# Kernel tuning notes

Hardware: AMD Instinct MI355X
Metric: run time of the kernel (lower is better)

Reference implementation:

```python
import jax, jax.numpy as jnp
import numpy as np

N_NODES = 50000
N_EDGES = 800000
NUM_GRAPHS = 512
EMB = 128
OUT_DIM = 2145 * 2
EPS_BN = 1e-5
EPS_GN = 1e-5


def gat_conv(x, src, dst, W, att_s, att_d, bias, n):
    # PyG GATConv, heads=1: h = x W ; alpha_e = leakyrelu(a_s.h[src] + a_d.h[dst])
    h = x @ W                                   # [N, EMB]
    a_s = h @ att_s                             # [N]
    a_d = h @ att_d                             # [N]
    logits = jax.nn.leaky_relu(a_s[src] + a_d[dst], 0.2)   # [E]
    m = jax.ops.segment_max(logits, dst, num_segments=n)
    ex = jnp.exp(logits - m[dst])
    denom = jax.ops.segment_sum(ex, dst, num_segments=n)
    alpha = ex / (denom[dst] + 1e-16)           # segment softmax over in-edges
    out = jax.ops.segment_sum(alpha[:, None] * h[src], dst, num_segments=n)
    return out + bias


def setup_inputs() -> dict:
    key = jax.random.key(0)
    ks = jax.random.split(key, 16)
    x = jax.random.normal(ks[0], (N_NODES, 1), dtype=jnp.float32)
    edge_index = jax.random.randint(ks[1], (2, N_EDGES), 0, N_NODES, dtype=jnp.int64)
    batch = jnp.sort(jax.random.randint(ks[2], (N_NODES,), 0, NUM_GRAPHS, dtype=jnp.int64))
    edge_attr = jax.random.normal(ks[3], (N_EDGES, 1), dtype=jnp.float32)
    s = 0.1
    return {
        "x": x, "edge_index": edge_index, "batch": batch, "edge_attr": edge_attr,
        "W0": jax.random.normal(ks[4], (1, EMB), dtype=jnp.float32) * s,
        "as0": jax.random.normal(ks[5], (EMB,), dtype=jnp.float32) * s,
        "ad0": jax.random.normal(ks[6], (EMB,), dtype=jnp.float32) * s,
        "b0": jnp.zeros((EMB,), dtype=jnp.float32),
        "W1": jax.random.normal(ks[7], (EMB, EMB), dtype=jnp.float32) * s,
        "as1": jax.random.normal(ks[8], (EMB,), dtype=jnp.float32) * s,
        "ad1": jax.random.normal(ks[9], (EMB,), dtype=jnp.float32) * s,
        "b1": jnp.zeros((EMB,), dtype=jnp.float32),
        "bn_g": jnp.ones((EMB,), dtype=jnp.float32),
        "bn_b": jnp.zeros((EMB,), dtype=jnp.float32),
        "gn_w": jnp.ones((EMB,), dtype=jnp.float32),
        "gn_b": jnp.zeros((EMB,), dtype=jnp.float32),
        "gn_ms": jnp.ones((EMB,), dtype=jnp.float32),
        "Wout": jax.random.normal(ks[10], (2 * EMB, OUT_DIM), dtype=jnp.float32) * s,
        "bout": jnp.zeros((OUT_DIM,), dtype=jnp.float32),
    }


def reference(x, edge_index, batch, edge_attr, W0, as0, ad0, b0, W1, as1, ad1, b1,
              bn_g, bn_b, gn_w, gn_b, gn_ms, Wout, bout):
    n = x.shape[0]
    # PyG GATConv add_self_loops=True
    loops = jnp.arange(n, dtype=edge_index.dtype)
    src = jnp.concatenate([edge_index[0], loops])
    dst = jnp.concatenate([edge_index[1], loops])
    # edge_attr ignored (edge_dim=None in GATConv)

    h = jnp.tanh(gat_conv(x, src, dst, W0, as0, ad0, b0, n))
    # dropout p=0.2 treated as identity (deterministic eval reference)

    # BatchNorm over nodes (training/batch statistics)
    mu = jnp.mean(h, axis=0)
    var = jnp.mean((h - mu) ** 2, axis=0)
    h = bn_g * (h - mu) / jnp.sqrt(var + EPS_BN) + bn_b

    # GraphNorm: per-graph mean-scale normalization
    cnt = jax.ops.segment_sum(jnp.ones((n,), h.dtype), batch, num_segments=NUM_GRAPHS)[:, None]
    gmean = jax.ops.segment_sum(h, batch, num_segments=NUM_GRAPHS) / cnt
    h0 = h - gmean[batch] * gn_ms
    gvar = jax.ops.segment_sum(h0 ** 2, batch, num_segments=NUM_GRAPHS) / cnt
    h = gn_w * h0 / jnp.sqrt(gvar[batch] + EPS_GN) + gn_b

    h = jnp.tanh(gat_conv(h, src, dst, W1, as1, ad1, b1, n))

    # global max + mean pool per graph
    pmax = jax.ops.segment_max(h, batch, num_segments=NUM_GRAPHS)
    pmean = jax.ops.segment_sum(h, batch, num_segments=NUM_GRAPHS) / cnt
    pooled = jnp.concatenate([pmax, pmean], axis=1)   # [G, 2*EMB]
    return pooled @ Wout + bout                        # [G, OUT_DIM]
```

## Files before the change

### kernel.cpp

```cpp
#include <hip/hip_runtime.h>
#include <hip/hip_fp16.h>
#include <math.h>

#define EMB 128
#define NGRAPH 512
#define MAXBUCK 800
#define BCAP 1536
#define CHUNK 8192

typedef _Float16 f16_t;
typedef _Float16 f16x8 __attribute__((ext_vector_type(8)));
typedef float f32x4 __attribute__((ext_vector_type(4)));

__device__ __forceinline__ float leaky(float v){ return v > 0.f ? v : 0.2f*v; }
__device__ __forceinline__ float ftanh(float x){
    float u = __expf(2.f*x);
    return 1.f - 2.f*__builtin_amdgcn_rcpf(u + 1.f);
}
__device__ __forceinline__ float frcp(float x){ return __builtin_amdgcn_rcpf(x); }

__global__ __launch_bounds__(256) void k_misc(const float* W0, const float* as0, const float* ad0,
                                              float* c_sd, const float* W1, f16_t* W1t,
                                              const float* Wout, int OUT, f16_t* WoutT){
    __shared__ f16_t lt[64*68];
    __shared__ float s1[128], s2[128];
    int b = blockIdx.x;
    int t = threadIdx.x;
    if(b < 272){
        int n0 = (b%68)*64, k0 = (b/68)*64;
        #pragma unroll
        for(int j=0;j<16;j++){
            int k_l = (t>>6)*16 + j;
            int n_l = t&63;
            int n = n0+n_l;
            float v = (n < OUT) ? Wout[(size_t)(k0+k_l)*OUT + n] : 0.f;
            lt[n_l*68 + k_l] = (f16_t)v;
        }
        __syncthreads();
        #pragma unroll
        for(int j=0;j<16;j++){
            int n_l = (t>>6)*16 + j;
            int k_l = t&63;
            WoutT[(size_t)(n0+n_l)*256 + k0 + k_l] = lt[n_l*68 + k_l];
        }
    } else if(b < 336){
        int idx = (b-272)*256 + t;
        int n = idx>>7, k = idx&127;
        W1t[n*128+k] = (f16_t)W1[k*128+n];
    } else {
        if(t<128){ float w = W0[t]; s1[t]=w*as0[t]; s2[t]=w*ad0[t]; }
        __syncthreads();
        for(int off=64; off>0; off>>=1){
            if(t<off){ s1[t]+=s1[t+off]; s2[t]+=s2[t+off]; }
            __syncthreads();
        }
        if(t==0){ c_sd[0]=s1[0]; c_sd[1]=s2[0]; }
    }
}

__global__ void k_bcount(const int* dst, int E, int nbuck, int* bcnt){
    __shared__ int h[MAXBUCK];
    int t = threadIdx.x;
    for(int j=t;j<MAXBUCK;j+=512) h[j]=0;
    __syncthreads();
    int stride = gridDim.x*blockDim.x;
    for(int e = blockIdx.x*blockDim.x+t; e<E; e+=stride)
        atomicAdd(&h[dst[e]>>6], 1);
    __syncthreads();
    for(int j=t;j<nbuck;j+=512) if(h[j]) atomicAdd(&bcnt[j], h[j]);
}

__global__ void k_bscan(const int* bcnt, int nbuck, int* bbase, int* bcursor,
                        const int* batch, int N, int* gstart){
    __shared__ int s[1024];
    int t = threadIdx.x;
    int own = (t<nbuck)? bcnt[t] : 0;
    s[t] = own;
    __syncthreads();
    for(int off=1; off<1024; off<<=1){
        int a = (t>=off)? s[t-off] : 0;
        __syncthreads();
        s[t] += a;
        __syncthreads();
    }
    if(t<nbuck){ int ex = s[t]-own; bbase[t]=ex; bcursor[t]=ex; }
    if(t==nbuck-1) bbase[nbuck]=s[t];
    for(int i=t; i<N; i+=1024){
        int b2 = batch[i];
        if(i==0){ for(int g=0;g<=b2;g++) gstart[g]=0; }
        else { int bp=batch[i-1]; for(int g=bp+1; g<=b2; g++) gstart[g]=i; }
        if(i==N-1){ for(int g=b2+1; g<=NGRAPH; g++) gstart[g]=N; }
    }
}

__global__ __launch_bounds__(512) void k_bscatter(const int* src, const int* dst, int E,
                                                  int nbuck, int* bcursor, unsigned* ebuf){
    __shared__ int cnt[MAXBUCK];
    __shared__ int loff[MAXBUCK];
    __shared__ int cur[MAXBUCK];
    __shared__ int gbase[MAXBUCK];
    __shared__ int s[1024];
    __shared__ unsigned srt[CHUNK];
    int t = threadIdx.x;
    int c0 = blockIdx.x*CHUNK;
    int m = E - c0; if(m > CHUNK) m = CHUNK;
    for(int j=t;j<MAXBUCK;j+=512) cnt[j]=0;
    __syncthreads();
    unsigned rec[16];
    #pragma unroll
    for(int u=0;u<16;u++){
        int j = u*512 + t;
        if(j<m){
            int d = dst[c0+j];
            int sv = src[c0+j];
            rec[u] = ((unsigned)(d>>6)<<22) | ((unsigned)(d&63)<<16) | (unsigned)sv;
            atomicAdd(&cnt[d>>6], 1);
        } else rec[u] = 0xFFFFFFFFu;
    }
    __syncthreads();
    int v0 = (t<nbuck)? cnt[t]:0;
    int j2 = t+512;
    int v1 = (j2<nbuck)? cnt[j2]:0;
    s[t]=v0; s[j2]=v1;
    __syncthreads();
    for(int off=1; off<1024; off<<=1){
        int a = (t>=off)? s[t-off]:0;
        int b = s[j2-off];
        __syncthreads();
        s[t]+=a; s[j2]+=b;
        __syncthreads();
    }
    for(int j=t;j<nbuck;j+=512){
        int c = cnt[j];
        int ex = s[j]-c;
        loff[j]=ex; cur[j]=ex;
        if(c>0) gbase[j]=atomicAdd(&bcursor[j], c);
    }
    __syncthreads();
    #pragma unroll
    for(int u=0;u<16;u++){
        if(rec[u]!=0xFFFFFFFFu){
            int b = rec[u]>>22;
            int p = atomicAdd(&cur[b],1);
            srt[p]=rec[u];
        }
    }
    __syncthreads();
    for(int j=t;j<m;j+=512){
        unsigned r = srt[j];
        int b = r>>22;
        ebuf[gbase[b] + (j - loff[b])] = r;
    }
}

__global__ __launch_bounds__(256) void k_gat0(const unsigned* ebuf, const int* bbase,
                                              const float* x, const float* c_sd,
                                              int N, float* s0,
                                              unsigned short* csr16, int* rowstart){
    __shared__ unsigned raw[BCAP];
    __shared__ unsigned short esrc[BCAP];
    __shared__ int cnt[64], off[64], cur[64];
    int t = threadIdx.x;
    int b = blockIdx.x;
    int e0 = bbase[b];
    int m = bbase[b+1]-e0; if(m>BCAP) m=BCAP;
    for(int j=t;j<m;j+=256) raw[j]=ebuf[e0+j];
    if(t<64) cnt[t]=0;
    __syncthreads();
    for(int j=t;j<m;j+=256) atomicAdd(&cnt[(raw[j]>>16)&63],1);
    __syncthreads();
    if(t<64){
        int v = cnt[t]; int inc = v;
        #pragma unroll
        for(int o=1;o<64;o<<=1){ int u = __shfl_up(inc,o); if(t>=o) inc+=u; }
        off[t]=inc-v; cur[t]=inc-v;
    }
    __syncthreads();
    for(int j=t;j<m;j+=256){
        unsigned r=raw[j]; int n=(r>>16)&63;
        int p=atomicAdd(&cur[n],1);
        esrc[p]=(unsigned short)(r&0xFFFF);
    }
    __syncthreads();
    for(int j=t;j<m;j+=256) csr16[e0+j]=esrc[j];
    if(t<64) rowstart[b*64+t] = e0 + off[t];
    int n = t>>2, sub = t&3;
    int gid = b*64 + n;
    if(gid>=N) return;
    float cs=c_sd[0], cd=c_sd[1];
    float xi = x[gid]; float adi = cd*xi;
    int r0=off[n], r1=cur[n];
    float den=0.f, num=0.f;
    if(sub==0){
        float ex = __expf(leaky(fmaf(cs,xi,adi)));
        den=ex; num=ex*xi;
    }
    for(int e=r0+sub;e<r1;e+=4){
        float xs = x[esrc[e]];
        float ee = __expf(leaky(fmaf(cs,xs,adi)));
        den += ee; num = fmaf(ee,xs,num);
    }
    den += __shfl_xor(den,1); den += __shfl_xor(den,2);
    num += __shfl_xor(num,1); num += __shfl_xor(num,2);
    if(sub==0) s0[gid] = num*frcp(den+1e-16f);
}

__global__ void k_gstats(const float* s0, const int* gstart, const float* W0, const float* b0,
                         float* gsum, float* gsumsq){
    int g=blockIdx.x, k=threadIdx.x;
    float wk=W0[k], bk=b0[k];
    int i0=gstart[g], i1=gstart[g+1];
    float s=0.f, q=0.f;
    for(int i=i0;i<i1;i++){
        float t=ftanh(fmaf(s0[i],wk,bk));
        s+=t; q=fmaf(t,t,q);
    }
    gsum[g*EMB+k]=s; gsumsq[g*EMB+k]=q;
}

__global__ void k_bnstats(const float* gsum, const float* gsumsq,
                          const float* bn_g, const float* bn_b, int N,
                          float* bnsc, float* bnsh){
    int k=threadIdx.x;
    float cs=0.f, cq=0.f;
    for(int g=0; g<NGRAPH; g++){ cs+=gsum[g*EMB+k]; cq+=gsumsq[g*EMB+k]; }
    float invN = 1.f/(float)N;
    float mu=cs*invN; float var = cq*invN - mu*mu;
    float sc = bn_g[k]*rsqrtf(var+1e-5f);
    bnsc[k]=sc; bnsh[k]=bn_b[k]-mu*sc;
}

__global__ void k_pq(const float* gsum, const float* gsumsq, const int* gstart,
                     const float* bnsc, const float* bnsh,
                     const float* gn_w, const float* gn_b, const float* gn_ms,
                     float* P, float* Q){
    int idx = blockIdx.x*blockDim.x+threadIdx.x;
    int g = idx>>7, k = idx&127;
    int c = gstart[g+1]-gstart[g];
    float rc = frcp((float)(c>0?c:1));
    float m1 = gsum[idx]*rc, m2 = gsumsq[idx]*rc;
    float A = bnsc[k], Bs = bnsh[k];
    float gmean = fmaf(A,m1,Bs);
    float B = Bs - gmean*gn_ms[k];
    float gvar = A*A*m2 + 2.f*A*B*m1 + B*B;
    float rg = rsqrtf(gvar+1e-5f);
    float w = gn_w[k];
    P[idx] = w*A*rg;
    Q[idx] = fmaf(w*B, rg, gn_b[k]);
}

__global__ __launch_bounds__(256) void k_gemm1(const float* s0, const int* batch,
        const float* W0, const float* b0, const float* P, const float* Q,
        const f16_t* W1t, const float* as1, const float* ad1,
        int N, f16_t* h1, float* a_s, float* a_d){
    __shared__ f16_t A_lds[64*128];
    __shared__ f16_t ob[64*136];
    int t = threadIdx.x;
    int i0 = blockIdx.x*64;
    #pragma unroll
    for(int j=0;j<4;j++){
        int c = t + 256*j;
        int r = c>>4, q = c&15;
        int i = i0 + r;
        f16x8 chunk;
        if(i < N){
            float s = s0[i]; int g = batch[i];
            int k0 = q*8;
            const float* Pg=&P[g*EMB+k0]; const float* Qg=&Q[g*EMB+k0];
            const float* W0p=&W0[k0]; const float* b0p=&b0[k0];
            #pragma unroll
            for(int u=0;u<8;u++)
                chunk[u] = (f16_t)fmaf(Pg[u], ftanh(fmaf(s,W0p[u],b0p[u])), Qg[u]);
        } else {
            #pragma unroll
            for(int u=0;u<8;u++) chunk[u] = (f16_t)0.f;
        }
        *(f16x8*)&A_lds[r*128 + ((q ^ (r&15))<<3)] = chunk;
    }
    __syncthreads();
    int w = t>>6, l = t&63;
    int lm = l&15, lq = l>>4;
    f16x8 a[4];
    #pragma unroll
    for(int kt=0;kt<4;kt++){
        int r = w*16 + lm;
        int q = kt*4 + lq;
        a[kt] = *(const f16x8*)&A_lds[r*128 + ((q ^ (r&15))<<3)];
    }
    f32x4 acc[8];
    #pragma unroll
    for(int nt=0;nt<8;nt++) acc[nt] = (f32x4){0.f,0.f,0.f,0.f};
    #pragma unroll
    for(int nt=0;nt<8;nt++){
        const f16_t* bp = &W1t[(nt*16 + lm)*128 + lq*8];
        f16x8 b0v = *(const f16x8*)&bp[0];
        f16x8 b1v = *(const f16x8*)&bp[32];
        f16x8 b2v = *(const f16x8*)&bp[64];
        f16x8 b3v = *(const f16x8*)&bp[96];
        acc[nt] = __builtin_amdgcn_mfma_f32_16x16x32_f16(a[0], b0v, acc[nt], 0, 0, 0);
        acc[nt] = __builtin_amdgcn_mfma_f32_16x16x32_f16(a[1], b1v, acc[nt], 0, 0, 0);
        acc[nt] = __builtin_amdgcn_mfma_f32_16x16x32_f16(a[2], b2v, acc[nt], 0, 0, 0);
        acc[nt] = __builtin_amdgcn_mfma_f32_16x16x32_f16(a[3], b3v, acc[nt], 0, 0, 0);
    }
    float ps[4] = {0.f,0.f,0.f,0.f};
    float pd[4] = {0.f,0.f,0.f,0.f};
    #pragma unroll
    for(int nt=0;nt<8;nt++){
        int n = nt*16 + lm;
        float asv = as1[n], adv = ad1[n];
        #pragma unroll
        for(int r=0;r<4;r++){
            ps[r] = fmaf(acc[nt][r], asv, ps[r]);
            pd[r] = fmaf(acc[nt][r], adv, pd[r]);
        }
    }
    #pragma unroll
    for(int r=0;r<4;r++){
        #pragma unroll
        for(int off=1; off<16; off<<=1){
            ps[r] += __shfl_xor(ps[r], off);
            pd[r] += __shfl_xor(pd[r], off);
        }
    }
    if(lm==0){
        #pragma unroll
        for(int r=0;r<4;r++){
            int i = i0 + w*16 + lq*4 + r;
            if(i < N){ a_s[i]=ps[r]; a_d[i]=pd[r]; }
        }
    }
    #pragma unroll
    for(int nt=0;nt<8;nt++){
        int n = nt*16 + lm;
        #pragma unroll
        for(int r=0;r<4;r++){
            int row = w*16 + lq*4 + r;
            ob[row*136 + n] = (f16_t)acc[nt][r];
        }
    }
    __syncthreads();
    #pragma unroll
    for(int c=0;c<4;c++){
        int idx = t + 256*c;
        int row = idx>>4, q = idx&15;
        int i = i0 + row;
        if(i < N){
            f16x8 v = *(const f16x8*)&ob[row*136 + q*8];
            *(f16x8*)&h1[(size_t)i*EMB + q*8] = v;
        }
    }
}

__global__ __launch_bounds__(256) void k_gat1(const unsigned short* csr16, const int* rowstart,
                                              const f16_t* h1, const float* a_s, const float* a_d,
                                              const float* b1, int N, f16_t* h2){
    int wave = threadIdx.x>>6, lane = threadIdx.x&63;
    int i = blockIdx.x*4 + wave;
    if(i>=N) return;
    int r0=rowstart[i], r1=rowstart[i+1]; int deg=r1-r0;
    float adi = a_d[i];
    float exs = __expf(leaky(a_s[i] + adi) - 4.f);
    const __half2* h1v = (const __half2*)h1;
    float2 hv = __half22float2(h1v[(size_t)i*64 + lane]);
    float2 acc0; acc0.x = exs*hv.x; acc0.y = exs*hv.y;
    float2 acc1 = {0.f,0.f}, acc2 = {0.f,0.f}, acc3 = {0.f,0.f};
    float denp = (lane==0)? exs : 0.f;
    for(int c=0;c<deg;c+=64){
        int e = c+lane;
        unsigned pk = 0;
        if(e<deg){
            int s = (int)csr16[r0+e];
            float ex = __expf(leaky(a_s[s]+adi)-4.f);
            denp += ex;
            pk = (unsigned)s | ((unsigned)__half_as_ushort(__float2half(ex))<<16);
        }
        int cnt = min(64, deg-c);
        int jj=0;
        for(; jj+7<cnt; jj+=8){
            unsigned p0=__shfl(pk,jj+0), p1=__shfl(pk,jj+1), p2=__shfl(pk,jj+2), p3=__shfl(pk,jj+3);
            unsigned p4=__shfl(pk,jj+4), p5=__shfl(pk,jj+5), p6=__shfl(pk,jj+6), p7=__shfl(pk,jj+7);
            float2 v0 = __half22float2(h1v[(size_t)(p0&0xFFFF)*64 + lane]);
            float2 v1 = __half22float2(h1v[(size_t)(p1&0xFFFF)*64 + lane]);
            float2 v2 = __half22float2(h1v[(size_t)(p2&0xFFFF)*64 + lane]);
            float2 v3 = __half22float2(h1v[(size_t)(p3&0xFFFF)*64 + lane]);
            float2 v4 = __half22float2(h1v[(size_t)(p4&0xFFFF)*64 + lane]);
            float2 v5 = __half22float2(h1v[(size_t)(p5&0xFFFF)*64 + lane]);
            float2 v6 = __half22float2(h1v[(size_t)(p6&0xFFFF)*64 + lane]);
            float2 v7 = __half22float2(h1v[(size_t)(p7&0xFFFF)*64 + lane]);
            float a0=__half2float(__ushort_as_half((unsigned short)(p0>>16)));
            float a1=__half2float(__ushort_as_half((unsigned short)(p1>>16)));
            float a2=__half2float(__ushort_as_half((unsigned short)(p2>>16)));
            float a3=__half2float(__ushort_as_half((unsigned short)(p3>>16)));
            float a4=__half2float(__ushort_as_half((unsigned short)(p4>>16)));
            float a5=__half2float(__ushort_as_half((unsigned short)(p5>>16)));
            float a6=__half2float(__ushort_as_half((unsigned short)(p6>>16)));
            float a7=__half2float(__ushort_as_half((unsigned short)(p7>>16)));
            acc0.x = fmaf(a0, v0.x, acc0.x); acc0.y = fmaf(a0, v0.y, acc0.y);
            acc1.x = fmaf(a1, v1.x, acc1.x); acc1.y = fmaf(a1, v1.y, acc1.y);
            acc2.x = fmaf(a2, v2.x, acc2.x); acc2.y = fmaf(a2, v2.y, acc2.y);
            acc3.x = fmaf(a3, v3.x, acc3.x); acc3.y = fmaf(a3, v3.y, acc3.y);
            acc0.x = fmaf(a4, v4.x, acc0.x); acc0.y = fmaf(a4, v4.y, acc0.y);
            acc1.x = fmaf(a5, v5.x, acc1.x); acc1.y = fmaf(a5, v5.y, acc1.y);
            acc2.x = fmaf(a6, v6.x, acc2.x); acc2.y = fmaf(a6, v6.y, acc2.y);
            acc3.x = fmaf(a7, v7.x, acc3.x); acc3.y = fmaf(a7, v7.y, acc3.y);
        }
        for(; jj<cnt; jj++){
            unsigned p0=__shfl(pk,jj);
            float2 v0 = __half22float2(h1v[(size_t)(p0&0xFFFF)*64 + lane]);
            float a0=__half2float(__ushort_as_half((unsigned short)(p0>>16)));
            acc0.x = fmaf(a0, v0.x, acc0.x); acc0.y = fmaf(a0, v0.y, acc0.y);
        }
    }
    acc0.x += acc1.x + acc2.x + acc3.x;
    acc0.y += acc1.y + acc2.y + acc3.y;
    for(int o=32; o; o>>=1) denp += __shfl_xor(denp, o);
    float rden = frcp(denp + 1e-16f);
    float2 bb = *(const float2*)&b1[lane*2];
    float ox = ftanh(fmaf(acc0.x, rden, bb.x));
    float oy = ftanh(fmaf(acc0.y, rden, bb.y));
    *(__half2*)&h2[(size_t)i*EMB + lane*2] = __floats2half2_rn(ox, oy);
}

__global__ void k_pool(const f16_t* h2, const int* gstart, f16_t* pooled){
    int g=blockIdx.x, k=threadIdx.x;
    const __half2* h2v = (const __half2*)h2;
    int i0=gstart[g], i1=gstart[g+1];
    float2 mx = {-1e30f,-1e30f}, sm = {0.f,0.f};
    for(int i=i0;i<i1;i++){
        float2 v=__half22float2(h2v[(size_t)i*64+k]);
        mx.x=fmaxf(mx.x,v.x); mx.y=fmaxf(mx.y,v.y);
        sm.x+=v.x; sm.y+=v.y;
    }
    float c = frcp((float)((i1-i0)>0 ? (i1-i0) : 1));
    pooled[g*256+2*k  ]=(f16_t)mx.x;
    pooled[g*256+2*k+1]=(f16_t)mx.y;
    pooled[g*256+128+2*k  ]=(f16_t)(sm.x*c);
    pooled[g*256+128+2*k+1]=(f16_t)(sm.y*c);
}

__global__ __launch_bounds__(256) void k_out(const f16_t* pooled, const f16_t* WoutT,
                                             const float* bout, int OUT, float* out){
    int t = threadIdx.x;
    int w = t>>6, l = t&63;
    int lm = l&15, lq = l>>4;
    int m0 = (blockIdx.y*4 + w)*16;
    int n0 = blockIdx.x*64;
    f16x8 a[8];
    const f16_t* ap = &pooled[(m0+lm)*256 + lq*8];
    #pragma unroll
    for(int kt=0;kt<8;kt++) a[kt] = *(const f16x8*)&ap[kt*32];
    f32x4 acc[4];
    #pragma unroll
    for(int nt=0;nt<4;nt++) acc[nt] = (f32x4){0.f,0.f,0.f,0.f};
    #pragma unroll
    for(int nt=0;nt<4;nt++){
        const f16_t* bp = &WoutT[(size_t)(n0 + nt*16 + lm)*256 + lq*8];
        #pragma unroll
        for(int kt=0;kt<8;kt++){
            f16x8 b = *(const f16x8*)&bp[kt*32];
            acc[nt] = __builtin_amdgcn_mfma_f32_16x16x32_f16(a[kt], b, acc[nt], 0, 0, 0);
        }
    }
    #pragma unroll
    for(int nt=0;nt<4;nt++){
        int n = n0 + nt*16 + lm;
        if(n >= OUT) continue;
        float bv = bout[n];
        #pragma unroll
        for(int r=0;r<4;r++){
            int m = m0 + lq*4 + r;
            out[(size_t)m*OUT + n] = acc[nt][r] + bv;
        }
    }
}

extern "C" void kernel_launch(void* const* d_in, const int* in_sizes, int n_in,
                              void* d_out, int out_size, void* d_ws, size_t ws_size,
                              hipStream_t stream) {
    const float* x    = (const float*)d_in[0];
    const int*   eidx = (const int*)d_in[1];
    const int*   batch= (const int*)d_in[2];
    const float* W0   = (const float*)d_in[4];
    const float* as0  = (const float*)d_in[5];
    const float* ad0  = (const float*)d_in[6];
    const float* b0   = (const float*)d_in[7];
    const float* W1   = (const float*)d_in[8];
    const float* as1  = (const float*)d_in[9];
    const float* ad1  = (const float*)d_in[10];
    const float* b1   = (const float*)d_in[11];
    const float* bn_g = (const float*)d_in[12];
    const float* bn_b = (const float*)d_in[13];
    const float* gn_w = (const float*)d_in[14];
    const float* gn_b = (const float*)d_in[15];
    const float* gn_ms= (const float*)d_in[16];
    const float* Wout = (const float*)d_in[17];
    const float* bout = (const float*)d_in[18];

    int N = in_sizes[0];
    int E = in_sizes[1]/2;
    int OUT = out_size / NGRAPH;
    const int* srcp = eidx;
    const int* dstp = eidx + E;
    int nbuck = (N+63)>>6;

    char* w = (char*)d_ws;
    auto alloc = [&](size_t bytes) -> void* {
        void* p = (void*)w; w += (bytes+255)&~(size_t)255; return p;
    };
    int* bcnt     = (int*)alloc(MAXBUCK*4);
    int* bbase    = (int*)alloc((MAXBUCK+1)*4);
    int* bcursor  = (int*)alloc(MAXBUCK*4);
    unsigned* ebuf= (unsigned*)alloc((size_t)E*4);
    unsigned short* csr16 = (unsigned short*)alloc((size_t)E*2);
    int* rowstart = (int*)alloc((size_t)(MAXBUCK*64+64)*4);
    float* c_sd   = (float*)alloc(256);
    float* s0     = (float*)alloc((size_t)N*4);
    int* gstart   = (int*)alloc((NGRAPH+1)*4);
    float* gsum   = (float*)alloc(NGRAPH*EMB*4);
    float* gsq    = (float*)alloc(NGRAPH*EMB*4);
    float* bnsc   = (float*)alloc(512);
    float* bnsh   = (float*)alloc(512);
    float* P      = (float*)alloc(NGRAPH*EMB*4);
    float* Q      = (float*)alloc(NGRAPH*EMB*4);
    f16_t* h1     = (f16_t*)alloc((size_t)N*EMB*2);
    f16_t* h2     = (f16_t*)alloc((size_t)N*EMB*2);
    float* a_sv   = (float*)alloc((size_t)N*4);
    float* a_dv   = (float*)alloc((size_t)N*4);
    f16_t* pooled = (f16_t*)alloc(NGRAPH*256*2);
    f16_t* w1t    = (f16_t*)alloc(128*128*2);
    f16_t* woutt  = (f16_t*)alloc((size_t)4352*256*2);

    hipMemsetAsync(bcnt, 0, MAXBUCK*4, stream);

    k_misc<<<337,256,0,stream>>>(W0,as0,ad0,c_sd,W1,w1t,Wout,OUT,woutt);
    k_bcount<<<120,512,0,stream>>>(dstp,E,nbuck,bcnt);
    k_bscan<<<1,1024,0,stream>>>(bcnt,nbuck,bbase,bcursor,batch,N,gstart);
    int nchunk = (E+CHUNK-1)/CHUNK;
    k_bscatter<<<nchunk,512,0,stream>>>(srcp,dstp,E,nbuck,bcursor,ebuf);
    k_gat0<<<nbuck,256,0,stream>>>(ebuf,bbase,x,c_sd,N,s0,csr16,rowstart);
    k_gstats<<<NGRAPH,128,0,stream>>>(s0,gstart,W0,b0,gsum,gsq);
    k_bnstats<<<1,128,0,stream>>>(gsum,gsq,bn_g,bn_b,N,bnsc,bnsh);
    k_pq<<<(NGRAPH*EMB)/256,256,0,stream>>>(gsum,gsq,gstart,bnsc,bnsh,gn_w,gn_b,gn_ms,P,Q);
    k_gemm1<<<(N+63)/64,256,0,stream>>>(s0,batch,W0,b0,P,Q,w1t,as1,ad1,N,h1,a_sv,a_dv);
    k_gat1<<<(N+3)/4,256,0,stream>>>(csr16,rowstart,h1,a_sv,a_dv,b1,N,h2);
    k_pool<<<NGRAPH,64,0,stream>>>(h2,gstart,pooled);
    dim3 og(68, 8);
    k_out<<<og,256,0,stream>>>(pooled,woutt,bout,OUT,(float*)d_out);
}
```

Baseline: 213.0 us.

## Split gstart build into parallel kernel and unfuse normalized-H production from GEMM

Moves the per-graph segment-start computation out of the single-block scan kernel into its own fully parallel kernel. It also splits the tanh/GraphNorm activation computation out of k_gemm1 into a separate grid-stride kernel that writes an fp16 H buffer. The GEMM then loads A fragments directly from global memory instead of staging them through LDS. This cuts the serial work in the one-block scan, but adds an extra N×128 fp16 write and read plus two more kernel launches.

```diff
diff --git a/kernel.cpp b/kernel.cpp
--- a/kernel.cpp
+++ b/kernel.cpp
@@ -70,8 +70,7 @@
     for(int j=t;j<nbuck;j+=512) if(h[j]) atomicAdd(&bcnt[j], h[j]);
 }
 
-__global__ void k_bscan(const int* bcnt, int nbuck, int* bbase, int* bcursor,
-                        const int* batch, int N, int* gstart){
+__global__ void k_bscan(const int* bcnt, int nbuck, int* bbase, int* bcursor){
     __shared__ int s[1024];
     int t = threadIdx.x;
     int own = (t<nbuck)? bcnt[t] : 0;
@@ -85,12 +84,15 @@
     }
     if(t<nbuck){ int ex = s[t]-own; bbase[t]=ex; bcursor[t]=ex; }
     if(t==nbuck-1) bbase[nbuck]=s[t];
-    for(int i=t; i<N; i+=1024){
-        int b2 = batch[i];
-        if(i==0){ for(int g=0;g<=b2;g++) gstart[g]=0; }
-        else { int bp=batch[i-1]; for(int g=bp+1; g<=b2; g++) gstart[g]=i; }
-        if(i==N-1){ for(int g=b2+1; g<=NGRAPH; g++) gstart[g]=N; }
-    }
+}
+
+__global__ void k_gseg(const int* batch, int N, int* gstart){
+    int i = blockIdx.x*blockDim.x+threadIdx.x;
+    if(i>=N) return;
+    int b = batch[i];
+    if(i==0){ for(int g=0;g<=b;g++) gstart[g]=0; }
+    else { int bp=batch[i-1]; for(int g=bp+1; g<=b; g++) gstart[g]=i; }
+    if(i==N-1){ for(int g=b+1; g<=NGRAPH; g++) gstart[g]=N; }
 }
 
 __global__ __launch_bounds__(512) void k_bscatter(const int* src, const int* dst, int E,
@@ -249,44 +251,38 @@
     Q[idx] = fmaf(w*B, rg, gn_b[k]);
 }
 
-__global__ __launch_bounds__(256) void k_gemm1(const float* s0, const int* batch,
-        const float* W0, const float* b0, const float* P, const float* Q,
-        const f16_t* W1t, const float* as1, const float* ad1,
+__global__ void k_H(const float* s0, const int* batch, const float* W0, const float* b0,
+                    const float* P, const float* Q, int N, f16_t* H){
+    int total = N*16;
+    int stride = gridDim.x*blockDim.x;
+    for(int idx = blockIdx.x*blockDim.x+threadIdx.x; idx < total; idx += stride){
+        int i = idx>>4;
+        int k0 = (idx&15)*8;
+        float s = s0[i]; int g = batch[i];
+        const float* Pg=&P[g*EMB+k0]; const float* Qg=&Q[g*EMB+k0];
+        const float* W0p=&W0[k0]; const float* b0p=&b0[k0];
+        f16x8 o;
+        #pragma unroll
+        for(int u=0;u<8;u++){
+            o[u] = (f16_t)fmaf(Pg[u], ftanh(fmaf(s,W0p[u],b0p[u])), Qg[u]);
+        }
+        *(f16x8*)&H[(size_t)i*EMB + k0] = o;
+    }
+}
+
+__global__ __launch_bounds__(256) void k_gemm1(const f16_t* H, const f16_t* W1t,
+        const float* as1, const float* ad1,
         int N, f16_t* h1, float* a_s, float* a_d){
-    __shared__ f16_t A_lds[64*128];
     __shared__ f16_t ob[64*136];
     int t = threadIdx.x;
     int i0 = blockIdx.x*64;
-    #pragma unroll
-    for(int j=0;j<4;j++){
-        int c = t + 256*j;
-        int r = c>>4, q = c&15;
-        int i = i0 + r;
-        f16x8 chunk;
-        if(i < N){
-            float s = s0[i]; int g = batch[i];
-            int k0 = q*8;
-            const float* Pg=&P[g*EMB+k0]; const float* Qg=&Q[g*EMB+k0];
-            const float* W0p=&W0[k0]; const float* b0p=&b0[k0];
-            #pragma unroll
-            for(int u=0;u<8;u++)
-                chunk[u] = (f16_t)fmaf(Pg[u], ftanh(fmaf(s,W0p[u],b0p[u])), Qg[u]);
-        } else {
-            #pragma unroll
-            for(int u=0;u<8;u++) chunk[u] = (f16_t)0.f;
-        }
-        *(f16x8*)&A_lds[r*128 + ((q ^ (r&15))<<3)] = chunk;
-    }
-    __syncthreads();
     int w = t>>6, l = t&63;
     int lm = l&15, lq = l>>4;
+    int arow = i0 + w*16 + lm; if(arow > N-1) arow = N-1;
+    const f16_t* ap = &H[(size_t)arow*EMB + lq*8];
     f16x8 a[4];
     #pragma unroll
-    for(int kt=0;kt<4;kt++){
-        int r = w*16 + lm;
-        int q = kt*4 + lq;
-        a[kt] = *(const f16x8*)&A_lds[r*128 + ((q ^ (r&15))<<3)];
-    }
+    for(int kt=0;kt<4;kt++) a[kt] = *(const f16x8*)&ap[kt*32];
     f32x4 acc[8];
     #pragma unroll
     for(int nt=0;nt<8;nt++) acc[nt] = (f32x4){0.f,0.f,0.f,0.f};
@@ -522,6 +518,7 @@
     float* bnsh   = (float*)alloc(512);
     float* P      = (float*)alloc(NGRAPH*EMB*4);
     float* Q      = (float*)alloc(NGRAPH*EMB*4);
+    f16_t* Hbuf   = (f16_t*)alloc((size_t)N*EMB*2);
     f16_t* h1     = (f16_t*)alloc((size_t)N*EMB*2);
     f16_t* h2     = (f16_t*)alloc((size_t)N*EMB*2);
     float* a_sv   = (float*)alloc((size_t)N*4);
@@ -534,14 +531,16 @@
 
     k_misc<<<337,256,0,stream>>>(W0,as0,ad0,c_sd,W1,w1t,Wout,OUT,woutt);
     k_bcount<<<120,512,0,stream>>>(dstp,E,nbuck,bcnt);
-    k_bscan<<<1,1024,0,stream>>>(bcnt,nbuck,bbase,bcursor,batch,N,gstart);
+    k_bscan<<<1,1024,0,stream>>>(bcnt,nbuck,bbase,bcursor);
     int nchunk = (E+CHUNK-1)/CHUNK;
     k_bscatter<<<nchunk,512,0,stream>>>(srcp,dstp,E,nbuck,bcursor,ebuf);
+    k_gseg<<<(N+255)/256,256,0,stream>>>(batch,N,gstart);
     k_gat0<<<nbuck,256,0,stream>>>(ebuf,bbase,x,c_sd,N,s0,csr16,rowstart);
     k_gstats<<<NGRAPH,128,0,stream>>>(s0,gstart,W0,b0,gsum,gsq);
     k_bnstats<<<1,128,0,stream>>>(gsum,gsq,bn_g,bn_b,N,bnsc,bnsh);
     k_pq<<<(NGRAPH*EMB)/256,256,0,stream>>>(gsum,gsq,gstart,bnsc,bnsh,gn_w,gn_b,gn_ms,P,Q);
-    k_gemm1<<<(N+63)/64,256,0,stream>>>(s0,batch,W0,b0,P,Q,w1t,as1,ad1,N,h1,a_sv,a_dv);
+    k_H<<<1024,256,0,stream>>>(s0,batch,W0,b0,P,Q,N,Hbuf);
+    k_gemm1<<<(N+63)/64,256,0,stream>>>(Hbuf,w1t,as1,ad1,N,h1,a_sv,a_dv);
     k_gat1<<<(N+3)/4,256,0,stream>>>(csr16,rowstart,h1,a_sv,a_dv,b1,N,h2);
     k_pool<<<NGRAPH,64,0,stream>>>(h2,gstart,pooled);
     dim3 og(68, 8);
```

Measured after the change: 191.6 us. -10.1%, faster.
